# Kernel optimization log

Measured on AMD Instinct MI355X. Metric: run time of the kernel, lower is better.

## Reference

```python
import jax, jax.numpy as jnp
import numpy as np

B, STATE_DIM, REF_DIM, T, H, ACT_DIM = 2048, 32, 16, 100, 256, 2
IN_DIM = STATE_DIM + REF_DIM  # 48


def setup_inputs() -> dict:
    key = jax.random.key(0)
    ks = jax.random.split(key, 12)
    s = 1.0 / np.sqrt(H)  # PyTorch GRU init scale
    obs = jax.random.normal(ks[0], (B, STATE_DIM + T * REF_DIM), jnp.float32)
    u = lambda k, shape: jax.random.uniform(k, shape, jnp.float32, -s, s)
    return {
        "obs": obs,
        "w_ih_l0": u(ks[1], (3 * H, IN_DIM)),
        "w_hh_l0": u(ks[2], (3 * H, H)),
        "b_ih_l0": u(ks[3], (3 * H,)),
        "b_hh_l0": u(ks[4], (3 * H,)),
        "w_ih_l1": u(ks[5], (3 * H, H)),
        "w_hh_l1": u(ks[6], (3 * H, H)),
        "b_ih_l1": u(ks[7], (3 * H,)),
        "b_hh_l1": u(ks[8], (3 * H,)),
        "fc_w": u(ks[9], (ACT_DIM, H)),
        "fc_b": u(ks[10], (ACT_DIM,)),
        "act_high": jnp.ones((ACT_DIM,), jnp.float32),
        "act_low": -jnp.ones((ACT_DIM,), jnp.float32),
    }


def _gru_layer(x, w_ih, w_hh, b_ih, b_hh):
    # x: [B, T, D] -> outputs [B, T, H]; PyTorch GRU gate math (r, z, n order)
    h_dim = w_hh.shape[1]
    xg = jnp.einsum("btd,gd->btg", x, w_ih) + b_ih  # [B, T, 3H], precompute input gates

    def step(h, xg_t):
        hg = h @ w_hh.T + b_hh
        xr, xz, xn = jnp.split(xg_t, 3, axis=-1)
        hr, hz, hn = jnp.split(hg, 3, axis=-1)
        r = jax.nn.sigmoid(xr + hr)
        z = jax.nn.sigmoid(xz + hz)
        n = jnp.tanh(xn + r * hn)
        h_new = (1.0 - z) * n + z * h
        return h_new, h_new

    h0 = jnp.zeros((x.shape[0], h_dim), x.dtype)
    _, hs = jax.lax.scan(step, h0, jnp.swapaxes(xg, 0, 1))  # [T, B, H]
    return jnp.swapaxes(hs, 0, 1)


def reference(obs, w_ih_l0, w_hh_l0, b_ih_l0, b_hh_l0, w_ih_l1, w_hh_l1, b_ih_l1, b_hh_l1, fc_w, fc_b, act_high, act_low):
    state = obs[:, :STATE_DIM]                                  # [B, S]
    traj = obs[:, STATE_DIM:].reshape(obs.shape[0], -1, REF_DIM)  # [B, T, R]
    seq_len = traj.shape[1]
    state_exp = jnp.broadcast_to(state[:, None, :], (obs.shape[0], seq_len, STATE_DIM))
    x = jnp.concatenate([state_exp, traj], axis=2)              # [B, T, S+R]
    out = _gru_layer(x, w_ih_l0, w_hh_l0, b_ih_l0, b_hh_l0)
    out = _gru_layer(out, w_ih_l1, w_hh_l1, b_ih_l1, b_hh_l1)
    last = out[:, -1, :]                                        # [B, H]
    actions = last @ fc_w.T + fc_b                              # [B, A]
    return (act_high - act_low) / 2 * jnp.tanh(actions) + (act_high + act_low) / 2
```

## Files before the change

### kernel.cpp

```cpp
#include <hip/hip_runtime.h>
#include <hip/hip_bf16.h>
#include <stdint.h>
#include <stddef.h>


#define OBS_STRIDE 1632
#define H 256
#define M 16
#define THREADS 512

typedef __attribute__((ext_vector_type(8))) short bfrag8;
typedef __attribute__((ext_vector_type(4))) short bfrag4;
typedef __attribute__((ext_vector_type(4))) float floatx4;

#define MFMA16(a, b, c) __builtin_amdgcn_mfma_f32_16x16x32_bf16((a), (b), (c), 0, 0, 0)

__device__ __forceinline__ unsigned short f2bf(float f) {
  union { float f; unsigned int i; } v; v.f = f;
  unsigned int i = v.i + 0x7FFFu + ((v.i >> 16) & 1u);
  return (unsigned short)(i >> 16);
}
__device__ __forceinline__ float bf2f(unsigned short u) {
  union { unsigned int i; float f; } v; v.i = ((unsigned int)u) << 16; return v.f;
}
__device__ __forceinline__ float fsigm(float x) {
  return __builtin_amdgcn_rcpf(1.f + __builtin_amdgcn_exp2f(-1.44269504f * x));
}
__device__ __forceinline__ float ftanh(float x) {
  return 1.f - 2.f * __builtin_amdgcn_rcpf(1.f + __builtin_amdgcn_exp2f(2.88539008f * x));
}

__device__ __forceinline__ void ld16_async(bfrag8& d, const unsigned short* p) {
  asm volatile("global_load_dwordx4 %0, %1, off" : "=v"(d) : "v"(p));
}
__device__ __forceinline__ void wait6(bfrag8& a, bfrag8& b, bfrag8& c,
                                      bfrag8& d, bfrag8& e, bfrag8& f) {
  asm volatile("s_waitcnt vmcnt(0)"
               : "+v"(a), "+v"(b), "+v"(c), "+v"(d), "+v"(e), "+v"(f) :: "memory");
}

__global__ void k_prep(const float* __restrict__ wih0, const float* __restrict__ whh0,
                       const float* __restrict__ wih1, const float* __restrict__ whh1,
                       unsigned short* __restrict__ o_wihs, unsigned short* __restrict__ o_wihr,
                       unsigned short* __restrict__ o_whh0,
                       unsigned short* __restrict__ o_wih1, unsigned short* __restrict__ o_whh1,
                       float* __restrict__ h0, float* __restrict__ h1) {
  long idx = (long)blockIdx.x * blockDim.x + threadIdx.x;
  const long ns = 768L * 32, n1 = 768L * 256, nh = 2048L * 256;
  if (idx < ns) { long r = idx >> 5, c = idx & 31;
                  o_wihs[idx] = f2bf(wih0[r * 48 + c]); return; }
  idx -= ns;
  if (idx < ns) { long r = idx >> 5, c = idx & 31;
                  o_wihr[idx] = (c < 16) ? f2bf(wih0[r * 48 + 32 + c]) : (unsigned short)0; return; }
  idx -= ns;
  if (idx < n1) { o_whh0[idx] = f2bf(whh0[idx]); return; }
  idx -= n1;
  if (idx < n1) { o_wih1[idx] = f2bf(wih1[idx]); return; }
  idx -= n1;
  if (idx < n1) { o_whh1[idx] = f2bf(whh1[idx]); return; }
  idx -= n1;
  if (idx < nh) { h0[idx] = 0.f; return; }
  idx -= nh;
  if (idx < nh) { h1[idx] = 0.f; return; }
}

__global__ __launch_bounds__(THREADS, 2) void k_fused(
    const float* __restrict__ obs,
    const unsigned short* __restrict__ g_wihs,
    const unsigned short* __restrict__ g_wihr,
    const unsigned short* __restrict__ g_whh0,
    const float* __restrict__ b_ih0, const float* __restrict__ b_hh0,
    float* __restrict__ h0state,
    unsigned short* __restrict__ out0c,
    const unsigned short* __restrict__ xg1c,
    const unsigned short* __restrict__ g_whh1,
    const float* __restrict__ b_ih1, const float* __restrict__ b_hh1,
    float* __restrict__ h1state,
    const float* __restrict__ fc_w, const float* __restrict__ fc_b,
    const float* __restrict__ act_high, const float* __restrict__ act_low,
    float* __restrict__ dout,
    int t0, int Tc, int do_l0, int do_l1, int is_last) {
  __shared__ __align__(16) unsigned short s_mem[71936];

  const int tid = threadIdx.x;
  const int wv = tid >> 6, lane = tid & 63, ln = lane & 15, qd = lane >> 4;
  const int role = blockIdx.x >> 7;
  const int bblk = blockIdx.x & 127;
  const int b0 = bblk * M;

  if (role == 0) {
    if (!do_l0) return;
    unsigned short* s_whh6 = s_mem;
    unsigned short* s_whh7 = s_mem + 30720;
    unsigned short* s_hA   = s_mem + 61440;
    unsigned short* s_x    = s_mem + 69888;
    unsigned short* s_st   = s_mem + 70912;

    for (int i = tid * 8; i < 768 * 32; i += THREADS * 8) {
      int m = i >> 5, c = i & 31;
      *(bfrag8*)&s_whh6[m * 40 + c] = *(const bfrag8*)&g_whh0[m * 256 + 192 + c];
      *(bfrag8*)&s_whh7[m * 40 + c] = *(const bfrag8*)&g_whh0[m * 256 + 224 + c];
    }
    { int r = tid >> 5, c = tid & 31;
      s_st[tid] = f2bf(obs[(size_t)(b0 + r) * OBS_STRIDE + c]); }
    if (tid < 256) {
      int r = tid >> 4, c = tid & 15;
      s_x[r * 32 + c] = f2bf(obs[(size_t)(b0 + r) * OBS_STRIDE + 32 + (size_t)t0 * 16 + c]);
      s_x[r * 32 + 16 + c] = 0;
      s_x[512 + r * 32 + 16 + c] = 0;
    }

    bfrag8 wf[6][6];
#pragma unroll
    for (int ks = 0; ks < 6; ++ks) {
#pragma unroll
      for (int f = 0; f < 6; ++f) {
        int nt = (f >> 1) * 16 + 2 * wv + (f & 1);
        ld16_async(wf[f][ks], g_whh0 + (size_t)(nt * 16 + ln) * 256 + ks * 32 + qd * 8);
      }
      wait6(wf[0][ks], wf[1][ks], wf[2][ks], wf[3][ks], wf[4][ks], wf[5][ks]);
    }
    bfrag8 wir[6];
#pragma unroll
    for (int f = 0; f < 6; ++f) {
      int nt = (f >> 1) * 16 + 2 * wv + (f & 1);
      wir[f] = *(const bfrag8*)&g_wihr[(size_t)(nt * 16 + ln) * 32 + qd * 8];
    }
    float bias_hn[2];
#pragma unroll
    for (int p = 0; p < 2; ++p) bias_hn[p] = b_hh0[512 + wv * 32 + p * 16 + ln];

    float h[2][4];
#pragma unroll
    for (int p = 0; p < 2; ++p)
#pragma unroll
      for (int i = 0; i < 4; ++i)
        h[p][i] = h0state[(size_t)(b0 + qd * 4 + i) * H + wv * 32 + p * 16 + ln];

    __syncthreads();

    floatx4 cc[6];
    {
      bfrag8 a_st = *(const bfrag8*)&s_st[ln * 32 + qd * 8];
#pragma unroll
      for (int f = 0; f < 6; ++f) {
        int nt = (f >> 1) * 16 + 2 * wv + (f & 1);
        int m = nt * 16 + ln;
        bfrag8 b_st = *(const bfrag8*)&g_wihs[(size_t)m * 32 + qd * 8];
        cc[f] = MFMA16(a_st, b_st, ((floatx4){0.f, 0.f, 0.f, 0.f}));
        float badd = b_ih0[m] + ((f < 4) ? b_hh0[m] : 0.f);
#pragma unroll
        for (int i = 0; i < 4; ++i) cc[f][i] += badd;
      }
    }
#pragma unroll
    for (int p = 0; p < 2; ++p)
#pragma unroll
      for (int i = 0; i < 4; ++i)
        s_hA[(qd * 4 + i) * 264 + wv * 32 + p * 16 + ln] = f2bf(h[p][i]);
    __syncthreads();

    const int orow = tid >> 5, ocol = (tid & 31) * 8;
    for (int tt = 0; tt < Tc; ++tt) {
      const int cur = tt & 1, nxt = cur ^ 1;
      if (tt > 0) {
        bfrag8 hv = *(const bfrag8*)&s_hA[cur * 4224 + orow * 264 + ocol];
        *(bfrag8*)&out0c[((size_t)(tt - 1) * 2048 + b0 + orow) * 256 + ocol] = hv;
      }
      float nref = 0.f;
      {
        int tl = (tt + 1 < Tc) ? tt + 1 : tt;
        if (tid < 256)
          nref = obs[(size_t)(b0 + (tid >> 4)) * OBS_STRIDE + 32 +
                     (size_t)(t0 + tl) * 16 + (tid & 15)];
      }

      floatx4 C[8];
#pragma unroll
      for (int f = 0; f < 6; ++f) C[f] = cc[f];
      C[6] = (floatx4){0.f, 0.f, 0.f, 0.f};
      C[7] = (floatx4){0.f, 0.f, 0.f, 0.f};

      {
        bfrag8 ax = *(const bfrag8*)&s_x[cur * 512 + ln * 32 + qd * 8];
        C[0] = MFMA16(ax, wir[0], C[0]);
        C[1] = MFMA16(ax, wir[1], C[1]);
        C[2] = MFMA16(ax, wir[2], C[2]);
        C[3] = MFMA16(ax, wir[3], C[3]);
        C[4] = MFMA16(ax, wir[4], C[4]);
        C[5] = MFMA16(ax, wir[5], C[5]);
      }
#pragma unroll
      for (int ks = 0; ks < 6; ++ks) {
        bfrag8 ah = *(const bfrag8*)&s_hA[cur * 4224 + ln * 264 + ks * 32 + qd * 8];
        C[0] = MFMA16(ah, wf[0][ks], C[0]);
        C[1] = MFMA16(ah, wf[1][ks], C[1]);
        C[2] = MFMA16(ah, wf[2][ks], C[2]);
        C[3] = MFMA16(ah, wf[3][ks], C[3]);
        C[6] = MFMA16(ah, wf[4][ks], C[6]);
        C[7] = MFMA16(ah, wf[5][ks], C[7]);
      }
      {
        bfrag8 ah = *(const bfrag8*)&s_hA[cur * 4224 + ln * 264 + 192 + qd * 8];
#pragma unroll
        for (int f = 0; f < 6; ++f) {
          int nt = (f >> 1) * 16 + 2 * wv + (f & 1);
          bfrag8 bh = *(const bfrag8*)&s_whh6[(nt * 16 + ln) * 40 + qd * 8];
          int ci = (f < 4) ? f : f + 2;
          C[ci] = MFMA16(ah, bh, C[ci]);
        }
      }
      {
        bfrag8 ah = *(const bfrag8*)&s_hA[cur * 4224 + ln * 264 + 224 + qd * 8];
#pragma unroll
        for (int f = 0; f < 6; ++f) {
          int nt = (f >> 1) * 16 + 2 * wv + (f & 1);
          bfrag8 bh = *(const bfrag8*)&s_whh7[(nt * 16 + ln) * 40 + qd * 8];
          int ci = (f < 4) ? f : f + 2;
          C[ci] = MFMA16(ah, bh, C[ci]);
        }
      }
#pragma unroll
      for (int p = 0; p < 2; ++p)
#pragma unroll
        for (int i = 0; i < 4; ++i) {
          float r = fsigm(C[0 + p][i]);
          float z = fsigm(C[2 + p][i]);
          float n = ftanh(C[4 + p][i] + r * (C[6 + p][i] + bias_hn[p]));
          h[p][i] = n + z * (h[p][i] - n);
          s_hA[nxt * 4224 + (qd * 4 + i) * 264 + wv * 32 + p * 16 + ln] = f2bf(h[p][i]);
        }
      if (tid < 256) s_x[nxt * 512 + (tid >> 4) * 32 + (tid & 15)] = f2bf(nref);
      __syncthreads();
    }
    {
      const int fb = Tc & 1;
      bfrag8 hv = *(const bfrag8*)&s_hA[fb * 4224 + orow * 264 + ocol];
      *(bfrag8*)&out0c[((size_t)(Tc - 1) * 2048 + b0 + orow) * 256 + ocol] = hv;
    }
#pragma unroll
    for (int p = 0; p < 2; ++p)
#pragma unroll
      for (int i = 0; i < 4; ++i)
        h0state[(size_t)(b0 + qd * 4 + i) * H + wv * 32 + p * 16 + ln] = h[p][i];

  } else {
    if (!do_l1) return;
    unsigned short* s_whh7 = s_mem;
    unsigned short* s_hA   = s_mem + 30720;

    for (int i = tid * 8; i < 768 * 32; i += THREADS * 8) {
      int m = i >> 5, c = i & 31;
      *(bfrag8*)&s_whh7[m * 40 + c] = *(const bfrag8*)&g_whh1[m * 256 + 224 + c];
    }
    bfrag8 wf[6][7];
#pragma unroll
    for (int ks = 0; ks < 7; ++ks) {
#pragma unroll
      for (int f = 0; f < 6; ++f) {
        int nt = (f >> 1) * 16 + 2 * wv + (f & 1);
        ld16_async(wf[f][ks], g_whh1 + (size_t)(nt * 16 + ln) * 256 + ks * 32 + qd * 8);
      }
      wait6(wf[0][ks], wf[1][ks], wf[2][ks], wf[3][ks], wf[4][ks], wf[5][ks]);
    }
    float bias_r[2], bias_z[2], bias_xn[2], bias_hn[2];
#pragma unroll
    for (int p = 0; p < 2; ++p) {
      int col = wv * 32 + p * 16 + ln;
      bias_r[p] = b_ih1[col] + b_hh1[col];
      bias_z[p] = b_ih1[256 + col] + b_hh1[256 + col];
      bias_xn[p] = b_ih1[512 + col];
      bias_hn[p] = b_hh1[512 + col];
    }
    float h[2][4];
#pragma unroll
    for (int p = 0; p < 2; ++p)
#pragma unroll
      for (int i = 0; i < 4; ++i)
        h[p][i] = h1state[(size_t)(b0 + qd * 4 + i) * H + wv * 32 + p * 16 + ln];
#pragma unroll
    for (int p = 0; p < 2; ++p)
#pragma unroll
      for (int i = 0; i < 4; ++i)
        s_hA[(qd * 4 + i) * 264 + wv * 32 + p * 16 + ln] = f2bf(h[p][i]);

    size_t offx[2][3];
#pragma unroll
    for (int p = 0; p < 2; ++p) {
      int col = wv * 32 + p * 16 + ln;
#pragma unroll
      for (int g = 0; g < 3; ++g)
        offx[p][g] = (size_t)(g * 256 + col) * 16 + qd * 4;
    }
    bfrag4 xr[2], xz[2], xn[2];
    {
      const unsigned short* xb = xg1c + (size_t)bblk * (768 * 16);
#pragma unroll
      for (int p = 0; p < 2; ++p) {
        xr[p] = *(const bfrag4*)&xb[offx[p][0]];
        xz[p] = *(const bfrag4*)&xb[offx[p][1]];
        xn[p] = *(const bfrag4*)&xb[offx[p][2]];
      }
    }
    __syncthreads();

    for (int tt = 0; tt < Tc; ++tt) {
      const int cur = tt & 1, nxt = cur ^ 1;
      bfrag4 nxr[2], nxz[2], nxn[2];
      {
        int tl = (tt + 1 < Tc) ? tt + 1 : tt;
        const unsigned short* xb = xg1c + ((size_t)tl * 128 + bblk) * (768 * 16);
#pragma unroll
        for (int p = 0; p < 2; ++p) {
          nxr[p] = *(const bfrag4*)&xb[offx[p][0]];
          nxz[p] = *(const bfrag4*)&xb[offx[p][1]];
          nxn[p] = *(const bfrag4*)&xb[offx[p][2]];
        }
      }

      floatx4 C[6];
#pragma unroll
      for (int i = 0; i < 6; ++i) C[i] = (floatx4){0.f, 0.f, 0.f, 0.f};
#pragma unroll
      for (int ks = 0; ks < 7; ++ks) {
        bfrag8 ah = *(const bfrag8*)&s_hA[cur * 4224 + ln * 264 + ks * 32 + qd * 8];
        C[0] = MFMA16(ah, wf[0][ks], C[0]);
        C[1] = MFMA16(ah, wf[1][ks], C[1]);
        C[2] = MFMA16(ah, wf[2][ks], C[2]);
        C[3] = MFMA16(ah, wf[3][ks], C[3]);
        C[4] = MFMA16(ah, wf[4][ks], C[4]);
        C[5] = MFMA16(ah, wf[5][ks], C[5]);
      }
      {
        bfrag8 ah = *(const bfrag8*)&s_hA[cur * 4224 + ln * 264 + 224 + qd * 8];
#pragma unroll
        for (int f = 0; f < 6; ++f) {
          int nt = (f >> 1) * 16 + 2 * wv + (f & 1);
          bfrag8 bh = *(const bfrag8*)&s_whh7[(nt * 16 + ln) * 40 + qd * 8];
          C[f] = MFMA16(ah, bh, C[f]);
        }
      }
#pragma unroll
      for (int p = 0; p < 2; ++p)
#pragma unroll
        for (int i = 0; i < 4; ++i) {
          float r = fsigm(C[0 + p][i] + bf2f((unsigned short)xr[p][i]) + bias_r[p]);
          float z = fsigm(C[2 + p][i] + bf2f((unsigned short)xz[p][i]) + bias_z[p]);
          float n = ftanh(bf2f((unsigned short)xn[p][i]) + bias_xn[p] +
                          r * (C[4 + p][i] + bias_hn[p]));
          h[p][i] = n + z * (h[p][i] - n);
          s_hA[nxt * 4224 + (qd * 4 + i) * 264 + wv * 32 + p * 16 + ln] = f2bf(h[p][i]);
        }
#pragma unroll
      for (int p = 0; p < 2; ++p) { xr[p] = nxr[p]; xz[p] = nxz[p]; xn[p] = nxn[p]; }
      __syncthreads();
    }
#pragma unroll
    for (int p = 0; p < 2; ++p)
#pragma unroll
      for (int i = 0; i < 4; ++i)
        h1state[(size_t)(b0 + qd * 4 + i) * H + wv * 32 + p * 16 + ln] = h[p][i];

    if (is_last) {
      const int fb = Tc & 1;
      int r = tid >> 5, a = (tid >> 4) & 1, kseg = tid & 15;
      float acc = 0.f;
#pragma unroll
      for (int j = 0; j < 16; ++j) {
        int k = kseg * 16 + j;
        acc += bf2f(s_hA[fb * 4224 + r * 264 + k]) * fc_w[a * H + k];
      }
      acc += __shfl_down(acc, 8);
      acc += __shfl_down(acc, 4);
      acc += __shfl_down(acc, 2);
      acc += __shfl_down(acc, 1);
      if (kseg == 0) {
        acc += fc_b[a];
        float hi = act_high[a], lo = act_low[a];
        float th = ftanh(acc);
        dout[(size_t)(b0 + r) * 2 + a] = 0.5f * (hi - lo) * th + 0.5f * (hi + lo);
      }
    }
  }
}

__global__ __launch_bounds__(THREADS, 2) void k_xg1(
    const unsigned short* __restrict__ out0c,
    const unsigned short* __restrict__ g_wih1,
    unsigned short* __restrict__ xg1c,
    int Tc) {
  const int tid = threadIdx.x;
  const int wv = tid >> 6, lane = tid & 63, ln = lane & 15, qd = lane >> 4;
  const int tt = blockIdx.x >> 3;
  const int b0 = (blockIdx.x & 7) * 256;

  bfrag8 af[6][8];
#pragma unroll
  for (int ks = 0; ks < 8; ++ks) {
#pragma unroll
    for (int f = 0; f < 6; ++f) {
      ld16_async(af[f][ks],
                 g_wih1 + (size_t)((wv * 6 + f) * 16 + ln) * 256 + ks * 32 + qd * 8);
    }
    wait6(af[0][ks], af[1][ks], af[2][ks], af[3][ks], af[4][ks], af[5][ks]);
  }
  for (int bt = 0; bt < 16; ++bt) {
    const int bb = b0 + bt * 16;
    floatx4 C[6];
#pragma unroll
    for (int f = 0; f < 6; ++f) C[f] = (floatx4){0.f, 0.f, 0.f, 0.f};
    const unsigned short* brow = out0c + ((size_t)tt * 2048 + bb + ln) * 256 + qd * 8;
#pragma unroll
    for (int ks = 0; ks < 8; ++ks) {
      bfrag8 bfr = *(const bfrag8*)(brow + ks * 32);
#pragma unroll
      for (int f = 0; f < 6; ++f) C[f] = MFMA16(af[f][ks], bfr, C[f]);
    }
    const size_t obase = ((size_t)tt * 128 + (bb >> 4)) * (768 * 16);
#pragma unroll
    for (int f = 0; f < 6; ++f) {
      int nt = wv * 6 + f;
#pragma unroll
      for (int i = 0; i < 4; ++i) {
        int m = nt * 16 + qd * 4 + i;
        xg1c[obase + (size_t)m * 16 + ln] = f2bf(C[f][i]);
      }
    }
  }
}

extern "C" void kernel_launch(void* const* d_in, const int* in_sizes, int n_in,
                              void* d_out, int out_size, void* d_ws, size_t ws_size,
                              hipStream_t stream) {
  const float* obs  = (const float*)d_in[0];
  const float* wih0 = (const float*)d_in[1];
  const float* whh0 = (const float*)d_in[2];
  const float* bih0 = (const float*)d_in[3];
  const float* bhh0 = (const float*)d_in[4];
  const float* wih1 = (const float*)d_in[5];
  const float* whh1 = (const float*)d_in[6];
  const float* bih1 = (const float*)d_in[7];
  const float* bhh1 = (const float*)d_in[8];
  const float* fcw  = (const float*)d_in[9];
  const float* fcb  = (const float*)d_in[10];
  const float* ahigh= (const float*)d_in[11];
  const float* alow = (const float*)d_in[12];

  char* ws = (char*)d_ws;
  unsigned short* ws_wihs = (unsigned short*)(ws + 0);
  unsigned short* ws_wihr = (unsigned short*)(ws + 49152);
  unsigned short* ws_whh0 = (unsigned short*)(ws + 98304);
  unsigned short* ws_wih1 = (unsigned short*)(ws + 491520);
  unsigned short* ws_whh1 = (unsigned short*)(ws + 884736);
  float* h0 = (float*)(ws + 1277952);
  float* h1 = (float*)(ws + 3375104);
  const size_t base = 5472256;

  int Tc = 1;
  const int cands[7] = {25, 20, 10, 5, 4, 2, 1};
  for (int i = 0; i < 7; ++i) {
    size_t need = base + (size_t)4194304 * cands[i];
    if (need <= ws_size) { Tc = cands[i]; break; }
  }
  unsigned short* out0c = (unsigned short*)(ws + base);
  unsigned short* xg1c  = (unsigned short*)(ws + base + (size_t)1048576 * Tc);
  const int nc = 100 / Tc;

  const long total_prep = 2 * 768L * 32 + 3 * 768L * 256 + 2 * 2048L * 256;
  k_prep<<<(int)((total_prep + 255) / 256), 256, 0, stream>>>(
      wih0, whh0, wih1, whh1, ws_wihs, ws_wihr, ws_whh0, ws_wih1, ws_whh1, h0, h1);

  for (int c = 0; c <= nc; ++c) {
    k_fused<<<256, THREADS, 0, stream>>>(
        obs, ws_wihs, ws_wihr, ws_whh0, bih0, bhh0, h0, out0c,
        xg1c, ws_whh1, bih1, bhh1, h1, fcw, fcb, ahigh, alow, (float*)d_out,
        c * Tc, Tc, (c < nc) ? 1 : 0, (c > 0) ? 1 : 0, (c == nc) ? 1 : 0);
    if (c < nc)
      k_xg1<<<Tc * 8, THREADS, 0, stream>>>(out0c, ws_wih1, xg1c, Tc);
  }
}
```

Baseline: 650.9 us.

## Double-buffer B tiles through LDS in xg1 kernel and lighten recurrent barriers

The input-projection kernel for layer 1 now loads each 16-row block of layer-0 output cooperatively into a double-buffered LDS tile. The next block is prefetched while the current one runs MFMAs, and the global stores of the previous tile's results are deferred so they overlap. Before, each wave re-read B fragments from global memory. The recurrent loops replace __syncthreads with an explicit lgkmcnt wait plus s_barrier, which avoids waiting on outstanding vector memory ops. The hand-counted vmcnt(24) wait depends on the exact number of outstanding stores and is fragile.

Result: slower. 689.6 us (+5.9%).

```diff
diff --git a/kernel.cpp b/kernel.cpp
--- a/kernel.cpp
+++ b/kernel.cpp
@@ -37,6 +37,15 @@
                                       bfrag8& d, bfrag8& e, bfrag8& f) {
   asm volatile("s_waitcnt vmcnt(0)"
                : "+v"(a), "+v"(b), "+v"(c), "+v"(d), "+v"(e), "+v"(f) :: "memory");
+}
+__device__ __forceinline__ void wait_vm0(bfrag8& a) {
+  asm volatile("s_waitcnt vmcnt(0)" : "+v"(a) :: "memory");
+}
+__device__ __forceinline__ void wait_vm24(bfrag8& a) {
+  asm volatile("s_waitcnt vmcnt(24)" : "+v"(a) :: "memory");
+}
+__device__ __forceinline__ void barrier_lgkm() {
+  asm volatile("s_waitcnt lgkmcnt(0)\n\ts_barrier" ::: "memory");
 }
 
 __global__ void k_prep(const float* __restrict__ wih0, const float* __restrict__ whh0,
@@ -231,7 +240,7 @@
           s_hA[nxt * 4224 + (qd * 4 + i) * 264 + wv * 32 + p * 16 + ln] = f2bf(h[p][i]);
         }
       if (tid < 256) s_x[nxt * 512 + (tid >> 4) * 32 + (tid & 15)] = f2bf(nref);
-      __syncthreads();
+      barrier_lgkm();
     }
     {
       const int fb = Tc & 1;
@@ -353,7 +362,7 @@
         }
 #pragma unroll
       for (int p = 0; p < 2; ++p) { xr[p] = nxr[p]; xz[p] = nxz[p]; xn[p] = nxn[p]; }
-      __syncthreads();
+      barrier_lgkm();
     }
 #pragma unroll
     for (int p = 0; p < 2; ++p)
@@ -389,6 +398,8 @@
     const unsigned short* __restrict__ g_wih1,
     unsigned short* __restrict__ xg1c,
     int Tc) {
+  __shared__ __align__(16) unsigned short s_b[2][16 * 264];
+
   const int tid = threadIdx.x;
   const int wv = tid >> 6, lane = tid & 63, ln = lane & 15, qd = lane >> 4;
   const int tt = blockIdx.x >> 3;
@@ -404,19 +415,56 @@
     }
     wait6(af[0][ks], af[1][ks], af[2][ks], af[3][ks], af[4][ks], af[5][ks]);
   }
+
+  const int srow = tid >> 5, scol = (tid & 31) * 8;
+  const unsigned short* gsrc = out0c + ((size_t)tt * 2048 + b0) * 256;
+
+  bfrag8 stg;
+  ld16_async(stg, gsrc + (size_t)srow * 256 + scol);
+  wait_vm0(stg);
+  *(bfrag8*)&s_b[0][srow * 264 + scol] = stg;
+  barrier_lgkm();
+
+  floatx4 C[6];
+#pragma unroll
+  for (int f = 0; f < 6; ++f) C[f] = (floatx4){0.f, 0.f, 0.f, 0.f};
+
   for (int bt = 0; bt < 16; ++bt) {
-    const int bb = b0 + bt * 16;
-    floatx4 C[6];
+    const int cur = bt & 1, nxt = cur ^ 1;
+    if (bt < 15)
+      ld16_async(stg, gsrc + ((size_t)(bt + 1) * 16 + srow) * 256 + scol);
+    if (bt > 0) {
+      const size_t obase = ((size_t)tt * 128 + ((b0 + (bt - 1) * 16) >> 4)) * (768 * 16);
+#pragma unroll
+      for (int f = 0; f < 6; ++f) {
+        int nt = wv * 6 + f;
+#pragma unroll
+        for (int i = 0; i < 4; ++i) {
+          int m = nt * 16 + qd * 4 + i;
+          xg1c[obase + (size_t)m * 16 + ln] = f2bf(C[f][i]);
+        }
+      }
+    }
 #pragma unroll
     for (int f = 0; f < 6; ++f) C[f] = (floatx4){0.f, 0.f, 0.f, 0.f};
-    const unsigned short* brow = out0c + ((size_t)tt * 2048 + bb + ln) * 256 + qd * 8;
 #pragma unroll
     for (int ks = 0; ks < 8; ++ks) {
-      bfrag8 bfr = *(const bfrag8*)(brow + ks * 32);
-#pragma unroll
-      for (int f = 0; f < 6; ++f) C[f] = MFMA16(af[f][ks], bfr, C[f]);
-    }
-    const size_t obase = ((size_t)tt * 128 + (bb >> 4)) * (768 * 16);
+      bfrag8 bfr = *(const bfrag8*)&s_b[cur][ln * 264 + ks * 32 + qd * 8];
+      C[0] = MFMA16(af[0][ks], bfr, C[0]);
+      C[1] = MFMA16(af[1][ks], bfr, C[1]);
+      C[2] = MFMA16(af[2][ks], bfr, C[2]);
+      C[3] = MFMA16(af[3][ks], bfr, C[3]);
+      C[4] = MFMA16(af[4][ks], bfr, C[4]);
+      C[5] = MFMA16(af[5][ks], bfr, C[5]);
+    }
+    if (bt < 15) {
+      if (bt == 0) wait_vm0(stg); else wait_vm24(stg);
+      *(bfrag8*)&s_b[nxt][srow * 264 + scol] = stg;
+    }
+    barrier_lgkm();
+  }
+  {
+    const size_t obase = ((size_t)tt * 128 + ((b0 + 15 * 16) >> 4)) * (768 * 16);
 #pragma unroll
     for (int f = 0; f < 6; ++f) {
       int nt = wv * 6 + f;
```

## Fold layer-1 input projection into fused kernel with double-buffered layer-0 output

Applied to the files above, without the earlier changes.

Removes the separate k_xg1 launch per chunk and computes the layer-1 input-gate projection inside the layer-1 role blocks at the start of each chunk, reading the previous chunk's layer-0 outputs. Layer-0 outputs are now ping-ponged between two buffers, so the layer-0 role can write chunk c while the layer-1 role reads chunk c-1 in the same launch. This cuts a kernel launch and a serialization point per chunk. The cost is extra work on the layer-1 blocks before their recurrence starts, plus a larger workspace, which may force a smaller chunk size. Block barriers are also replaced by an inline-asm barrier that waits only on LDS counters rather than doing a full sync.

Result: slower. 714.7 us (+9.8%).

```diff
diff --git a/kernel.cpp b/kernel.cpp
--- a/kernel.cpp
+++ b/kernel.cpp
@@ -37,6 +37,9 @@
                                       bfrag8& d, bfrag8& e, bfrag8& f) {
   asm volatile("s_waitcnt vmcnt(0)"
                : "+v"(a), "+v"(b), "+v"(c), "+v"(d), "+v"(e), "+v"(f) :: "memory");
+}
+__device__ __forceinline__ void barrier_lgkm() {
+  asm volatile("s_waitcnt lgkmcnt(0)\n\ts_barrier" ::: "memory");
 }
 
 __global__ void k_prep(const float* __restrict__ wih0, const float* __restrict__ whh0,
@@ -71,8 +74,10 @@
     const unsigned short* __restrict__ g_whh0,
     const float* __restrict__ b_ih0, const float* __restrict__ b_hh0,
     float* __restrict__ h0state,
-    unsigned short* __restrict__ out0c,
-    const unsigned short* __restrict__ xg1c,
+    unsigned short* __restrict__ out0w,
+    const unsigned short* __restrict__ out0r,
+    unsigned short* __restrict__ xg1c,
+    const unsigned short* __restrict__ g_wih1,
     const unsigned short* __restrict__ g_whh1,
     const float* __restrict__ b_ih1, const float* __restrict__ b_hh1,
     float* __restrict__ h1state,
@@ -165,7 +170,7 @@
       const int cur = tt & 1, nxt = cur ^ 1;
       if (tt > 0) {
         bfrag8 hv = *(const bfrag8*)&s_hA[cur * 4224 + orow * 264 + ocol];
-        *(bfrag8*)&out0c[((size_t)(tt - 1) * 2048 + b0 + orow) * 256 + ocol] = hv;
+        *(bfrag8*)&out0w[((size_t)(tt - 1) * 2048 + b0 + orow) * 256 + ocol] = hv;
       }
       float nref = 0.f;
       {
@@ -231,12 +236,12 @@
           s_hA[nxt * 4224 + (qd * 4 + i) * 264 + wv * 32 + p * 16 + ln] = f2bf(h[p][i]);
         }
       if (tid < 256) s_x[nxt * 512 + (tid >> 4) * 32 + (tid & 15)] = f2bf(nref);
-      __syncthreads();
+      barrier_lgkm();
     }
     {
       const int fb = Tc & 1;
       bfrag8 hv = *(const bfrag8*)&s_hA[fb * 4224 + orow * 264 + ocol];
-      *(bfrag8*)&out0c[((size_t)(Tc - 1) * 2048 + b0 + orow) * 256 + ocol] = hv;
+      *(bfrag8*)&out0w[((size_t)(Tc - 1) * 2048 + b0 + orow) * 256 + ocol] = hv;
     }
 #pragma unroll
     for (int p = 0; p < 2; ++p)
@@ -248,6 +253,45 @@
     if (!do_l1) return;
     unsigned short* s_whh7 = s_mem;
     unsigned short* s_hA   = s_mem + 30720;
+
+    {
+      bfrag8 af[6][8];
+#pragma unroll
+      for (int ks = 0; ks < 8; ++ks) {
+#pragma unroll
+        for (int f = 0; f < 6; ++f) {
+          ld16_async(af[f][ks],
+                     g_wih1 + (size_t)((wv * 6 + f) * 16 + ln) * 256 + ks * 32 + qd * 8);
+        }
+        wait6(af[0][ks], af[1][ks], af[2][ks], af[3][ks], af[4][ks], af[5][ks]);
+      }
+      for (int tt = 0; tt < Tc; ++tt) {
+        const unsigned short* brow = out0r + ((size_t)tt * 2048 + b0 + ln) * 256 + qd * 8;
+        floatx4 Cx[6];
+#pragma unroll
+        for (int f = 0; f < 6; ++f) Cx[f] = (floatx4){0.f, 0.f, 0.f, 0.f};
+#pragma unroll
+        for (int ks = 0; ks < 8; ++ks) {
+          bfrag8 bfr = *(const bfrag8*)(brow + ks * 32);
+          Cx[0] = MFMA16(af[0][ks], bfr, Cx[0]);
+          Cx[1] = MFMA16(af[1][ks], bfr, Cx[1]);
+          Cx[2] = MFMA16(af[2][ks], bfr, Cx[2]);
+          Cx[3] = MFMA16(af[3][ks], bfr, Cx[3]);
+          Cx[4] = MFMA16(af[4][ks], bfr, Cx[4]);
+          Cx[5] = MFMA16(af[5][ks], bfr, Cx[5]);
+        }
+        const size_t obase = ((size_t)tt * 128 + bblk) * (768 * 16);
+#pragma unroll
+        for (int f = 0; f < 6; ++f) {
+          int nt = wv * 6 + f;
+#pragma unroll
+          for (int i = 0; i < 4; ++i) {
+            int m = nt * 16 + qd * 4 + i;
+            xg1c[obase + (size_t)m * 16 + ln] = f2bf(Cx[f][i]);
+          }
+        }
+      }
+    }
 
     for (int i = tid * 8; i < 768 * 32; i += THREADS * 8) {
       int m = i >> 5, c = i & 31;
@@ -353,7 +397,7 @@
         }
 #pragma unroll
       for (int p = 0; p < 2; ++p) { xr[p] = nxr[p]; xz[p] = nxz[p]; xn[p] = nxn[p]; }
-      __syncthreads();
+      barrier_lgkm();
     }
 #pragma unroll
     for (int p = 0; p < 2; ++p)
@@ -379,51 +423,6 @@
         float hi = act_high[a], lo = act_low[a];
         float th = ftanh(acc);
         dout[(size_t)(b0 + r) * 2 + a] = 0.5f * (hi - lo) * th + 0.5f * (hi + lo);
-      }
-    }
-  }
-}
-
-__global__ __launch_bounds__(THREADS, 2) void k_xg1(
-    const unsigned short* __restrict__ out0c,
-    const unsigned short* __restrict__ g_wih1,
-    unsigned short* __restrict__ xg1c,
-    int Tc) {
-  const int tid = threadIdx.x;
-  const int wv = tid >> 6, lane = tid & 63, ln = lane & 15, qd = lane >> 4;
-  const int tt = blockIdx.x >> 3;
-  const int b0 = (blockIdx.x & 7) * 256;
-
-  bfrag8 af[6][8];
-#pragma unroll
-  for (int ks = 0; ks < 8; ++ks) {
-#pragma unroll
-    for (int f = 0; f < 6; ++f) {
-      ld16_async(af[f][ks],
-                 g_wih1 + (size_t)((wv * 6 + f) * 16 + ln) * 256 + ks * 32 + qd * 8);
-    }
-    wait6(af[0][ks], af[1][ks], af[2][ks], af[3][ks], af[4][ks], af[5][ks]);
-  }
-  for (int bt = 0; bt < 16; ++bt) {
-    const int bb = b0 + bt * 16;
-    floatx4 C[6];
-#pragma unroll
-    for (int f = 0; f < 6; ++f) C[f] = (floatx4){0.f, 0.f, 0.f, 0.f};
-    const unsigned short* brow = out0c + ((size_t)tt * 2048 + bb + ln) * 256 + qd * 8;
-#pragma unroll
-    for (int ks = 0; ks < 8; ++ks) {
-      bfrag8 bfr = *(const bfrag8*)(brow + ks * 32);
-#pragma unroll
-      for (int f = 0; f < 6; ++f) C[f] = MFMA16(af[f][ks], bfr, C[f]);
-    }
-    const size_t obase = ((size_t)tt * 128 + (bb >> 4)) * (768 * 16);
-#pragma unroll
-    for (int f = 0; f < 6; ++f) {
-      int nt = wv * 6 + f;
-#pragma unroll
-      for (int i = 0; i < 4; ++i) {
-        int m = nt * 16 + qd * 4 + i;
-        xg1c[obase + (size_t)m * 16 + ln] = f2bf(C[f][i]);
       }
     }
   }
@@ -459,11 +458,12 @@
   int Tc = 1;
   const int cands[7] = {25, 20, 10, 5, 4, 2, 1};
   for (int i = 0; i < 7; ++i) {
-    size_t need = base + (size_t)4194304 * cands[i];
+    size_t need = base + (size_t)5242880 * cands[i];
     if (need <= ws_size) { Tc = cands[i]; break; }
   }
-  unsigned short* out0c = (unsigned short*)(ws + base);
-  unsigned short* xg1c  = (unsigned short*)(ws + base + (size_t)1048576 * Tc);
+  unsigned short* out0A = (unsigned short*)(ws + base);
+  unsigned short* out0B = (unsigned short*)(ws + base + (size_t)1048576 * Tc);
+  unsigned short* xg1c  = (unsigned short*)(ws + base + (size_t)2097152 * Tc);
   const int nc = 100 / Tc;
 
   const long total_prep = 2 * 768L * 32 + 3 * 768L * 256 + 2 * 2048L * 256;
@@ -471,11 +471,12 @@
       wih0, whh0, wih1, whh1, ws_wihs, ws_wihr, ws_whh0, ws_wih1, ws_whh1, h0, h1);
 
   for (int c = 0; c <= nc; ++c) {
+    unsigned short* o0w = (c & 1) ? out0B : out0A;
+    const unsigned short* o0r = (c & 1) ? out0A : out0B;
     k_fused<<<256, THREADS, 0, stream>>>(
-        obs, ws_wihs, ws_wihr, ws_whh0, bih0, bhh0, h0, out0c,
-        xg1c, ws_whh1, bih1, bhh1, h1, fcw, fcb, ahigh, alow, (float*)d_out,
+        obs, ws_wihs, ws_wihr, ws_whh0, bih0, bhh0, h0, o0w, o0r,
+        xg1c, ws_wih1, ws_whh1, bih1, bhh1, h1,
+        fcw, fcb, ahigh, alow, (float*)d_out,
         c * Tc, Tc, (c < nc) ? 1 : 0, (c > 0) ? 1 : 0, (c == nc) ? 1 : 0);
-    if (c < nc)
-      k_xg1<<<Tc * 8, THREADS, 0, stream>>>(out0c, ws_wih1, xg1c, Tc);
   }
 }
```

## Split xg1 GEMM across more blocks, double-buffer activation loads, lighten barriers

Applied to the files above, without the earlier changes.

The layer-1 input-gate GEMM kernel now splits the gate dimension in half and the batch into 128-row slices, launching four times as many blocks, each holding fewer weight fragments. Activation fragments are prefetched into registers with a double buffer and a partial vmcnt wait, so global loads overlap the MFMAs. The recurrent loops swap __syncthreads for an explicit lgkmcnt(0) plus s_barrier, which avoids waiting on outstanding global memory ops. Each activation tile is now loaded by two blocks instead of one, and correctness depends on the hand-written waitcnt counts.

Result: slower. 797.4 us (+22.5%).

```diff
diff --git a/kernel.cpp b/kernel.cpp
--- a/kernel.cpp
+++ b/kernel.cpp
@@ -37,6 +37,21 @@
                                       bfrag8& d, bfrag8& e, bfrag8& f) {
   asm volatile("s_waitcnt vmcnt(0)"
                : "+v"(a), "+v"(b), "+v"(c), "+v"(d), "+v"(e), "+v"(f) :: "memory");
+}
+__device__ __forceinline__ void wait8_vm0(bfrag8& a, bfrag8& b, bfrag8& c, bfrag8& d,
+                                          bfrag8& e, bfrag8& f, bfrag8& g, bfrag8& h) {
+  asm volatile("s_waitcnt vmcnt(0)"
+               : "+v"(a), "+v"(b), "+v"(c), "+v"(d),
+                 "+v"(e), "+v"(f), "+v"(g), "+v"(h) :: "memory");
+}
+__device__ __forceinline__ void wait8_vm12(bfrag8& a, bfrag8& b, bfrag8& c, bfrag8& d,
+                                           bfrag8& e, bfrag8& f, bfrag8& g, bfrag8& h) {
+  asm volatile("s_waitcnt vmcnt(12)"
+               : "+v"(a), "+v"(b), "+v"(c), "+v"(d),
+                 "+v"(e), "+v"(f), "+v"(g), "+v"(h) :: "memory");
+}
+__device__ __forceinline__ void barrier_lgkm() {
+  asm volatile("s_waitcnt lgkmcnt(0)\n\ts_barrier" ::: "memory");
 }
 
 __global__ void k_prep(const float* __restrict__ wih0, const float* __restrict__ whh0,
@@ -231,7 +246,7 @@
           s_hA[nxt * 4224 + (qd * 4 + i) * 264 + wv * 32 + p * 16 + ln] = f2bf(h[p][i]);
         }
       if (tid < 256) s_x[nxt * 512 + (tid >> 4) * 32 + (tid & 15)] = f2bf(nref);
-      __syncthreads();
+      barrier_lgkm();
     }
     {
       const int fb = Tc & 1;
@@ -353,7 +368,7 @@
         }
 #pragma unroll
       for (int p = 0; p < 2; ++p) { xr[p] = nxr[p]; xz[p] = nxz[p]; xn[p] = nxn[p]; }
-      __syncthreads();
+      barrier_lgkm();
     }
 #pragma unroll
     for (int p = 0; p < 2; ++p)
@@ -391,41 +406,60 @@
     int Tc) {
   const int tid = threadIdx.x;
   const int wv = tid >> 6, lane = tid & 63, ln = lane & 15, qd = lane >> 4;
-  const int tt = blockIdx.x >> 3;
-  const int b0 = (blockIdx.x & 7) * 256;
-
-  bfrag8 af[6][8];
-#pragma unroll
-  for (int ks = 0; ks < 8; ++ks) {
-#pragma unroll
-    for (int f = 0; f < 6; ++f) {
-      ld16_async(af[f][ks],
-                 g_wih1 + (size_t)((wv * 6 + f) * 16 + ln) * 256 + ks * 32 + qd * 8);
-    }
-    wait6(af[0][ks], af[1][ks], af[2][ks], af[3][ks], af[4][ks], af[5][ks]);
-  }
-  for (int bt = 0; bt < 16; ++bt) {
-    const int bb = b0 + bt * 16;
-    floatx4 C[6];
-#pragma unroll
-    for (int f = 0; f < 6; ++f) C[f] = (floatx4){0.f, 0.f, 0.f, 0.f};
-    const unsigned short* brow = out0c + ((size_t)tt * 2048 + bb + ln) * 256 + qd * 8;
+  const int blk = blockIdx.x;
+  const int tt = blk >> 5;
+  const int bb = (blk >> 1) & 15;
+  const int gh = blk & 1;
+
+  bfrag8 af[3][8];
+#pragma unroll
+  for (int ks = 0; ks < 8; ++ks)
+#pragma unroll
+    for (int f = 0; f < 3; ++f) {
+      int nt = gh * 24 + wv * 3 + f;
+      ld16_async(af[f][ks], g_wih1 + (size_t)(nt * 16 + ln) * 256 + ks * 32 + qd * 8);
+    }
+  wait8_vm0(af[0][0], af[0][1], af[0][2], af[0][3], af[0][4], af[0][5], af[0][6], af[0][7]);
+  wait8_vm0(af[1][0], af[1][1], af[1][2], af[1][3], af[1][4], af[1][5], af[1][6], af[1][7]);
+  wait8_vm0(af[2][0], af[2][1], af[2][2], af[2][3], af[2][4], af[2][5], af[2][6], af[2][7]);
+
+  const unsigned short* gsrc = out0c + ((size_t)tt * 2048 + bb * 128 + ln) * 256 + qd * 8;
+
+  bfrag8 fr[2][8];
+#pragma unroll
+  for (int ks = 0; ks < 8; ++ks) ld16_async(fr[0][ks], gsrc + ks * 32);
+  wait8_vm0(fr[0][0], fr[0][1], fr[0][2], fr[0][3], fr[0][4], fr[0][5], fr[0][6], fr[0][7]);
+
+#pragma unroll
+  for (int bt = 0; bt < 8; ++bt) {
+    const int cur = bt & 1, nxt = cur ^ 1;
+    if (bt < 7) {
+      const unsigned short* nsrc = gsrc + (size_t)(bt + 1) * 16 * 256;
+#pragma unroll
+      for (int ks = 0; ks < 8; ++ks) ld16_async(fr[nxt][ks], nsrc + ks * 32);
+    }
+    floatx4 C[3];
+#pragma unroll
+    for (int f = 0; f < 3; ++f) C[f] = (floatx4){0.f, 0.f, 0.f, 0.f};
 #pragma unroll
     for (int ks = 0; ks < 8; ++ks) {
-      bfrag8 bfr = *(const bfrag8*)(brow + ks * 32);
-#pragma unroll
-      for (int f = 0; f < 6; ++f) C[f] = MFMA16(af[f][ks], bfr, C[f]);
-    }
-    const size_t obase = ((size_t)tt * 128 + (bb >> 4)) * (768 * 16);
-#pragma unroll
-    for (int f = 0; f < 6; ++f) {
-      int nt = wv * 6 + f;
+      C[0] = MFMA16(af[0][ks], fr[cur][ks], C[0]);
+      C[1] = MFMA16(af[1][ks], fr[cur][ks], C[1]);
+      C[2] = MFMA16(af[2][ks], fr[cur][ks], C[2]);
+    }
+    const size_t obase = ((size_t)tt * 128 + bb * 8 + bt) * (768 * 16);
+#pragma unroll
+    for (int f = 0; f < 3; ++f) {
+      int nt = gh * 24 + wv * 3 + f;
 #pragma unroll
       for (int i = 0; i < 4; ++i) {
         int m = nt * 16 + qd * 4 + i;
         xg1c[obase + (size_t)m * 16 + ln] = f2bf(C[f][i]);
       }
     }
+    if (bt < 7)
+      wait8_vm12(fr[nxt][0], fr[nxt][1], fr[nxt][2], fr[nxt][3],
+                 fr[nxt][4], fr[nxt][5], fr[nxt][6], fr[nxt][7]);
   }
 }
 
@@ -476,6 +510,6 @@
         xg1c, ws_whh1, bih1, bhh1, h1, fcw, fcb, ahigh, alow, (float*)d_out,
         c * Tc, Tc, (c < nc) ? 1 : 0, (c > 0) ? 1 : 0, (c == nc) ? 1 : 0);
     if (c < nc)
-      k_xg1<<<Tc * 8, THREADS, 0, stream>>>(out0c, ws_wih1, xg1c, Tc);
+      k_xg1<<<Tc * 32, THREADS, 0, stream>>>(out0c, ws_wih1, xg1c, Tc);
   }
 }
```
